# Optimization experiments

Hardware: AMD Instinct MI355X
Metric: run time of the kernel (lower is better)

Reference implementation:

```python
import jax, jax.numpy as jnp
import numpy as np

DEPTH = 4
CODEBOOK_NUM = 2048
CODEBOOK_DIM = 256


def setup_inputs() -> dict:
    key = jax.random.key(0)
    k1, k2 = jax.random.split(key)
    z = jax.random.normal(k1, (32, CODEBOOK_DIM, 32, 32), dtype=jnp.float32)
    # matches nn.init.uniform_(weight, -1/K, 1/K)
    codebook = jax.random.uniform(
        k2, (CODEBOOK_NUM, CODEBOOK_DIM), dtype=jnp.float32,
        minval=-1.0 / CODEBOOK_NUM, maxval=1.0 / CODEBOOK_NUM)
    return {"z": z, "codebook": codebook}


def _quantize(flat_z, codebook):
    # ||z||^2 + ||e||^2 - 2 z.e  -> [N, K]
    dists = (jnp.sum(flat_z ** 2, axis=1, keepdims=True)
             + jnp.sum(codebook ** 2, axis=1)
             - 2.0 * flat_z @ codebook.T)
    indices = jnp.argmin(dists, axis=1)          # [N]
    return codebook[indices], indices            # gather [N, C]


def reference(z, codebook):
    B, C, H, W = z.shape
    K = codebook.shape[0]
    residual = z
    q_list, idx_list = [], []
    for _ in range(DEPTH):
        flat = residual.transpose(0, 2, 3, 1).reshape(-1, C)   # [N, C]
        q_flat, idx = _quantize(flat, codebook)
        q = q_flat.reshape(B, H, W, C).transpose(0, 3, 1, 2)   # [B, C, H, W]
        q_list.append(q)
        idx_list.append(idx)
        residual = residual - q
    # prefix-sum across depth (matches the in-place accumulation loop)
    quantized_cum = jnp.cumsum(jnp.stack(q_list, axis=0), axis=0)  # [D,B,C,H,W]
    q_last = quantized_cum[-1]
    # note: residual here is z_orig - sum_q, so ST term is z_orig - 2*sum_q (faithful)
    quantized_z_st = q_last + jax.lax.stop_gradient(residual - q_last)
    all_idx = jnp.concatenate(idx_list, axis=0)                    # [D*N]
    # mean of one-hot == normalized histogram (avoids [D*N, K] materialization)
    counts = jnp.zeros((K,), dtype=jnp.float32).at[all_idx].add(1.0)
    probs = counts / all_idx.shape[0]
    perplexity = jnp.exp(-jnp.sum(probs * jnp.log(jnp.clip(probs, 1e-10))))
    indices = jnp.stack(idx_list, axis=0)                          # [D, N]
    return quantized_cum, quantized_z_st, indices, perplexity
```

## Files before the change

kernel.cpp:

```cpp
#include <hip/hip_runtime.h>
#include <math.h>

#define BB 32
#define CC 256
#define HWt 1024
#define NN 32768
#define KK 2048
#define RQDEPTH 4
#define CAP 64
#define DELTA 1e-3f

typedef __attribute__((ext_vector_type(8))) short short8;
typedef __attribute__((ext_vector_type(16))) float f32x16;

__device__ __forceinline__ float pw128sq(const float4* __restrict__ a4) {
  float r[8];
  {
    float4 p = a4[0], q = a4[1];
    r[0] = __fmul_rn(p.x, p.x); r[1] = __fmul_rn(p.y, p.y);
    r[2] = __fmul_rn(p.z, p.z); r[3] = __fmul_rn(p.w, p.w);
    r[4] = __fmul_rn(q.x, q.x); r[5] = __fmul_rn(q.y, q.y);
    r[6] = __fmul_rn(q.z, q.z); r[7] = __fmul_rn(q.w, q.w);
  }
  for (int i = 1; i < 16; ++i) {
    float4 p = a4[2 * i], q = a4[2 * i + 1];
    r[0] = __fadd_rn(r[0], __fmul_rn(p.x, p.x));
    r[1] = __fadd_rn(r[1], __fmul_rn(p.y, p.y));
    r[2] = __fadd_rn(r[2], __fmul_rn(p.z, p.z));
    r[3] = __fadd_rn(r[3], __fmul_rn(p.w, p.w));
    r[4] = __fadd_rn(r[4], __fmul_rn(q.x, q.x));
    r[5] = __fadd_rn(r[5], __fmul_rn(q.y, q.y));
    r[6] = __fadd_rn(r[6], __fmul_rn(q.z, q.z));
    r[7] = __fadd_rn(r[7], __fmul_rn(q.w, q.w));
  }
  return __fadd_rn(__fadd_rn(__fadd_rn(r[0], r[1]), __fadd_rn(r[2], r[3])),
                   __fadd_rn(__fadd_rn(r[4], r[5]), __fadd_rn(r[6], r[7])));
}

__device__ __forceinline__ unsigned short f2bf(float x) {
  unsigned u = __float_as_uint(x);
  return (unsigned short)((u + 0x7fffu + ((u >> 16) & 1u)) >> 16);
}
__device__ __forceinline__ unsigned fenc(float f) {
  unsigned u = __float_as_uint(f);
  return (u & 0x80000000u) ? ~u : (u | 0x80000000u);
}
__device__ __forceinline__ float fdec(unsigned k) {
  return __uint_as_float((k & 0x80000000u) ? (k ^ 0x80000000u) : ~k);
}

__global__ void k_ztrans(const float* __restrict__ z, float* __restrict__ resid) {
  __shared__ float tile[32][33];
  int b = blockIdx.z, c0 = blockIdx.y * 32, hw0 = blockIdx.x * 32;
  int tx = threadIdx.x & 31, ty = threadIdx.x >> 5;
  for (int i = ty; i < 32; i += 8)
    tile[i][tx] = z[((size_t)b * CC + c0 + i) * HWt + hw0 + tx];
  __syncthreads();
  for (int i = ty; i < 32; i += 8)
    resid[((size_t)b * HWt + hw0 + i) * CC + c0 + tx] = tile[tx][i];
}

__global__ void k_esplit(const float* __restrict__ cb, short8* __restrict__ esH8,
                         short8* __restrict__ esL8) {
  const int tg = blockIdx.x * 256 + threadIdx.x;
  const int k = tg >> 5, c8 = tg & 31;
  const int idx8 = ((k >> 5) * 32 + c8) * 32 + (k & 31);
  short8 H, L;
#pragma unroll
  for (int i = 0; i < 8; ++i) {
    float x = cb[(size_t)k * CC + c8 * 8 + i];
    unsigned short h = f2bf(x);
    float hf = __uint_as_float(((unsigned)h) << 16);
    unsigned short l = f2bf(__fsub_rn(x, hf));
    H[i] = (short)h; L[i] = (short)l;
  }
  esH8[idx8] = H; esL8[idx8] = L;
}

__global__ void k_bnorm(const float* __restrict__ cb, float* __restrict__ Bcol) {
  int k = blockIdx.x * 256 + threadIdx.x;
  if (k >= KK) return;
  const float4* row = (const float4*)(cb + (size_t)k * CC);
  Bcol[k] = __fadd_rn(pw128sq(row), pw128sq(row + 32));
}

__global__ void k_anorm(const float* __restrict__ resid, float* __restrict__ Arow) {
  int n = blockIdx.x * 256 + threadIdx.x;
  if (n >= NN) return;
  const float4* row = (const float4*)(resid + (size_t)n * CC);
  Arow[n] = __fadd_rn(pw128sq(row), pw128sq(row + 32));
}

__global__ void k_zero(int* counts) {
  int t = blockIdx.x * 256 + threadIdx.x;
  if (t < KK) counts[t] = 0;
}

__global__ __launch_bounds__(512, 4) void k_bulk(
    const float* __restrict__ resid, const short8* __restrict__ esH8,
    const short8* __restrict__ esL8, const float* __restrict__ cb,
    const float* __restrict__ Arow, const float* __restrict__ Bcol,
    int* __restrict__ idxAll, float* __restrict__ idxOut,
    int* __restrict__ counts, int depth) {
  __shared__ short8 zH8[32 * 32];
  __shared__ short8 zL8[32 * 32];
  __shared__ float zf[32 * 260];
  __shared__ int cnt[32];
  __shared__ unsigned minkey[32];
  __shared__ unsigned long long best[32];
  __shared__ int clist[32 * CAP];

  const int t = threadIdx.x;
  const int row0 = blockIdx.x * 32;

  if (t < 32) { cnt[t] = 0; minkey[t] = 0xFFFFFFFFu; best[t] = ~0ull; }

  {
    const int row = t >> 4;
    const int c4b = t & 15;
    const float4* src = (const float4*)(resid + (size_t)(row0 + row) * CC);
#pragma unroll
    for (int g = 0; g < 4; ++g) {
      const int c4i = c4b + 16 * g;
      *(float4*)(zf + row * 260 + c4i * 4) = src[c4i];
    }
  }
  __syncthreads();
  {
    const int srow = t & 31;
    const int c8a = (t >> 5) * 2;
#pragma unroll
    for (int cc = 0; cc < 2; ++cc) {
      const int c8 = c8a + cc;
      short8 H, L;
#pragma unroll
      for (int i = 0; i < 8; ++i) {
        float x = zf[srow * 260 + c8 * 8 + i];
        unsigned short h = f2bf(x);
        float hf = __uint_as_float(((unsigned)h) << 16);
        unsigned short l = f2bf(__fsub_rn(x, hf));
        H[i] = (short)h; L[i] = (short)l;
      }
      zH8[c8 * 32 + srow] = H;
      zL8[c8 * 32 + srow] = L;
    }
  }
  __syncthreads();

  const int wave = t >> 6, lane = t & 63;
  const int l31 = lane & 31, hh = lane >> 5;

#define LOADF(AH, AL, EH, EL, STEP)                                            \
  { const int o_ = ((STEP) * 2 + hh) * 32 + l31;                               \
    AH = zH8[o_]; AL = zL8[o_];                                                \
    EH = esH8[kt * 1024 + o_]; EL = esL8[kt * 1024 + o_]; }

#pragma unroll 1
  for (int it = 0; it < 8; ++it) {
    const int kt = wave * 8 + it, kb = kt * 32;
    f32x16 a0, a1;
#pragma unroll
    for (int i = 0; i < 16; ++i) { a0[i] = 0.f; a1[i] = 0.f; }

    short8 cah, cal, ceh, cel, nah, nal, neh, nel;
    LOADF(cah, cal, ceh, cel, 0)
#pragma unroll
    for (int step = 0; step < 16; ++step) {
      if (step < 15) LOADF(nah, nal, neh, nel, step + 1)
      a0 = __builtin_amdgcn_mfma_f32_32x32x16_bf16(cah, ceh, a0, 0, 0, 0);
      a1 = __builtin_amdgcn_mfma_f32_32x32x16_bf16(cah, cel, a1, 0, 0, 0);
      a1 = __builtin_amdgcn_mfma_f32_32x32x16_bf16(cal, ceh, a1, 0, 0, 0);
      __builtin_amdgcn_sched_barrier(0);
      if (step < 15) { cah = nah; cal = nal; ceh = neh; cel = nel; }
    }

    const float bkv = Bcol[kb + l31];
    float dt[16];
#pragma unroll
    for (int r = 0; r < 16; ++r) {
      const float m = __fadd_rn(a0[r], a1[r]);
      dt[r] = __fsub_rn(bkv, __fadd_rn(m, m));
    }
    if (it == 0) {
#pragma unroll
      for (int r = 0; r < 16; ++r) {
        float rm = dt[r];
#pragma unroll
        for (int m = 1; m < 32; m <<= 1) rm = fminf(rm, __shfl_xor(rm, m));
        if (l31 == 0) {
          const int rowr = (r & 3) + 8 * (r >> 2) + 4 * hh;
          atomicMin(&minkey[rowr], fenc(rm));
        }
      }
    }
#pragma unroll
    for (int r = 0; r < 16; ++r) {
      const int rowr = (r & 3) + 8 * (r >> 2) + 4 * hh;
      const float thr = fdec(minkey[rowr]) + DELTA;
      if (dt[r] <= thr) {
        atomicMin(&minkey[rowr], fenc(dt[r]));
        int idx = atomicAdd(&cnt[rowr], 1);
        if (idx < CAP) clist[rowr * CAP + idx] = kb + l31;
      }
    }
  }
  __syncthreads();

  {
    const int row = t >> 4;
    const int nc0 = cnt[row];
    const int nc = nc0 < CAP ? nc0 : CAP;
    const float av = Arow[row0 + row];
    const float* zr = zf + row * 260;
    for (int s = (t & 15); s < nc; s += 16) {
      const int k = clist[row * CAP + s];
      const float4* e4 = (const float4*)(cb + (size_t)k * CC);
      float a = 0.f;
#pragma unroll 8
      for (int c4 = 0; c4 < 64; ++c4) {
        const float4 z4 = *(const float4*)(zr + c4 * 4);
        const float4 q4 = e4[c4];
        a = fmaf(z4.x, q4.x, a);
        a = fmaf(z4.y, q4.y, a);
        a = fmaf(z4.z, q4.z, a);
        a = fmaf(z4.w, q4.w, a);
      }
      const float Cv = __fadd_rn(av, Bcol[k]);
      const float sv = __fsub_rn(Cv, __fadd_rn(a, a));
      unsigned long long pk =
          ((unsigned long long)__float_as_uint(sv) << 32) | (unsigned)k;
      atomicMin(&best[row], pk);
    }
  }
  __syncthreads();
  if (t < 32) {
    const int wi = (int)(unsigned)(best[t] & 0xffffffffu);
    const int n = row0 + t;
    idxAll[depth * NN + n] = wi;
    idxOut[n] = (float)wi;
    atomicAdd(counts + wi, 1);
  }
}

__global__ void k_update(const float* __restrict__ cb, const int* __restrict__ idxAll,
                         float* __restrict__ resid, float* __restrict__ cum,
                         float* __restrict__ zst, int depth) {
  __shared__ float qt[32][33];
  __shared__ float rt[32][33];
  int b = blockIdx.z, c0 = blockIdx.y * 32, hw0 = blockIdx.x * 32;
  int tx = threadIdx.x & 31, ty = threadIdx.x >> 5;
  const int* idx = idxAll + depth * NN;
  for (int i = ty; i < 32; i += 8) {
    int n = b * HWt + hw0 + i;
    int kk = idx[n];
    size_t fo = (size_t)n * CC + c0 + tx;
    float q = cb[(size_t)kk * CC + c0 + tx];
    float r = __fsub_rn(resid[fo], q);
    resid[fo] = r;
    qt[i][tx] = q;
    rt[i][tx] = r;
  }
  __syncthreads();
  const size_t PLANE = (size_t)NN * CC;
  for (int i = ty; i < 32; i += 8) {
    size_t oo = ((size_t)b * CC + c0 + i) * HWt + hw0 + tx;
    float q = qt[tx][i];
    float prevv = (depth == 0) ? 0.f : cum[(size_t)(depth - 1) * PLANE + oo];
    cum[(size_t)depth * PLANE + oo] = __fadd_rn(prevv, q);
    if (depth == 3) zst[oo] = rt[tx][i];
  }
}

__global__ void k_perp(const int* __restrict__ counts, float* __restrict__ out) {
  __shared__ double sh[256];
  double s = 0.0;
  for (int k = threadIdx.x; k < KK; k += 256) {
    int c = counts[k];
    if (c > 0) {
      double p = (double)c / (double)(RQDEPTH * NN);
      s += p * log(p);
    }
  }
  sh[threadIdx.x] = s;
  __syncthreads();
  for (int st = 128; st; st >>= 1) {
    if (threadIdx.x < st) sh[threadIdx.x] += sh[threadIdx.x + st];
    __syncthreads();
  }
  if (threadIdx.x == 0) out[0] = (float)exp(-sh[0]);
}

extern "C" void kernel_launch(void* const* d_in, const int* in_sizes, int n_in,
                              void* d_out, int out_size, void* d_ws, size_t ws_size,
                              hipStream_t stream) {
  const float* z  = (const float*)d_in[0];
  const float* cb = (const float*)d_in[1];
  float* out = (float*)d_out;
  const size_t PLANE = (size_t)NN * CC;
  float* cum  = out;
  float* zst  = out + (size_t)RQDEPTH * PLANE;
  float* idxo = zst + PLANE;
  float* perp = idxo + (size_t)RQDEPTH * NN;

  float* resid = (float*)d_ws;
  float* esbase = resid + PLANE;
  short8* esH8 = (short8*)esbase;
  short8* esL8 = esH8 + 65536;
  float* Arow  = esbase + (size_t)CC * KK;
  float* Bcol  = Arow + NN;
  int* idxAll  = (int*)(Bcol + KK);
  int* counts  = idxAll + RQDEPTH * NN;

  dim3 tgrid(HWt / 32, CC / 32, BB);
  k_ztrans<<<tgrid, 256, 0, stream>>>(z, resid);
  k_esplit<<<256, 256, 0, stream>>>(cb, esH8, esL8);
  k_bnorm<<<KK / 256, 256, 0, stream>>>(cb, Bcol);
  k_zero<<<(KK + 255) / 256, 256, 0, stream>>>(counts);

  for (int d = 0; d < RQDEPTH; ++d) {
    k_anorm<<<NN / 256, 256, 0, stream>>>(resid, Arow);
    k_bulk<<<NN / 32, 512, 0, stream>>>(resid, esH8, esL8, cb, Arow, Bcol,
                                        idxAll, idxo + (size_t)d * NN, counts, d);
    k_update<<<tgrid, 256, 0, stream>>>(cb, idxAll, resid, cum, zst, d);
  }
  k_perp<<<1, 256, 0, stream>>>(counts, perp);
}
```

Before: 946.4 us.

## Use single bf16 MFMA screening with wider margin and exact fp32 fallback

Drops the hi/lo bf16 split, so the candidate screen runs one bf16 MFMA per step instead of three. The shared-memory fp32 residual copy goes away and refinement reads the residual from global memory. The screening margin is raised to compensate for the coarser precision, and rows that overflow the candidate cap fall back to an exact scan over all codes. LDS shrinks enough to allow 8 blocks per CU. The risks are more candidates to refine per row, occasional full-scan fallbacks, and global-memory reads in the refine loop.

```diff
diff --git a/kernel.cpp b/kernel.cpp
--- a/kernel.cpp
+++ b/kernel.cpp
@@ -8,7 +8,7 @@
 #define KK 2048
 #define RQDEPTH 4
 #define CAP 64
-#define DELTA 1e-3f
+#define DELTA 4e-3f
 
 typedef __attribute__((ext_vector_type(8))) short short8;
 typedef __attribute__((ext_vector_type(16))) float f32x16;
@@ -49,6 +49,21 @@
   return __uint_as_float((k & 0x80000000u) ? (k ^ 0x80000000u) : ~k);
 }
 
+__device__ __forceinline__ float exact_dot(const float4* __restrict__ zr4,
+                                           const float4* __restrict__ e4) {
+  float a = 0.f;
+#pragma unroll 8
+  for (int c4 = 0; c4 < 64; ++c4) {
+    const float4 z4 = zr4[c4];
+    const float4 q4 = e4[c4];
+    a = fmaf(z4.x, q4.x, a);
+    a = fmaf(z4.y, q4.y, a);
+    a = fmaf(z4.z, q4.z, a);
+    a = fmaf(z4.w, q4.w, a);
+  }
+  return a;
+}
+
 __global__ void k_ztrans(const float* __restrict__ z, float* __restrict__ resid) {
   __shared__ float tile[32][33];
   int b = blockIdx.z, c0 = blockIdx.y * 32, hw0 = blockIdx.x * 32;
@@ -60,21 +75,18 @@
     resid[((size_t)b * HWt + hw0 + i) * CC + c0 + tx] = tile[tx][i];
 }
 
-__global__ void k_esplit(const float* __restrict__ cb, short8* __restrict__ esH8,
-                         short8* __restrict__ esL8) {
+__global__ void k_esplitH(const float* __restrict__ cb, short8* __restrict__ esH8) {
   const int tg = blockIdx.x * 256 + threadIdx.x;
   const int k = tg >> 5, c8 = tg & 31;
   const int idx8 = ((k >> 5) * 32 + c8) * 32 + (k & 31);
-  short8 H, L;
-#pragma unroll
-  for (int i = 0; i < 8; ++i) {
-    float x = cb[(size_t)k * CC + c8 * 8 + i];
-    unsigned short h = f2bf(x);
-    float hf = __uint_as_float(((unsigned)h) << 16);
-    unsigned short l = f2bf(__fsub_rn(x, hf));
-    H[i] = (short)h; L[i] = (short)l;
-  }
-  esH8[idx8] = H; esL8[idx8] = L;
+  const float4* s4 = (const float4*)(cb + (size_t)k * CC + c8 * 8);
+  float4 p = s4[0], q = s4[1];
+  short8 H;
+  H[0] = (short)f2bf(p.x); H[1] = (short)f2bf(p.y);
+  H[2] = (short)f2bf(p.z); H[3] = (short)f2bf(p.w);
+  H[4] = (short)f2bf(q.x); H[5] = (short)f2bf(q.y);
+  H[6] = (short)f2bf(q.z); H[7] = (short)f2bf(q.w);
+  esH8[idx8] = H;
 }
 
 __global__ void k_bnorm(const float* __restrict__ cb, float* __restrict__ Bcol) {
@@ -96,15 +108,12 @@
   if (t < KK) counts[t] = 0;
 }
 
-__global__ __launch_bounds__(512, 4) void k_bulk(
+__global__ __launch_bounds__(512, 8) void k_bulk(
     const float* __restrict__ resid, const short8* __restrict__ esH8,
-    const short8* __restrict__ esL8, const float* __restrict__ cb,
-    const float* __restrict__ Arow, const float* __restrict__ Bcol,
-    int* __restrict__ idxAll, float* __restrict__ idxOut,
-    int* __restrict__ counts, int depth) {
+    const float* __restrict__ cb, const float* __restrict__ Arow,
+    const float* __restrict__ Bcol, int* __restrict__ idxAll,
+    float* __restrict__ idxOut, int* __restrict__ counts, int depth) {
   __shared__ short8 zH8[32 * 32];
-  __shared__ short8 zL8[32 * 32];
-  __shared__ float zf[32 * 260];
   __shared__ int cnt[32];
   __shared__ unsigned minkey[32];
   __shared__ unsigned long long best[32];
@@ -116,33 +125,20 @@
   if (t < 32) { cnt[t] = 0; minkey[t] = 0xFFFFFFFFu; best[t] = ~0ull; }
 
   {
-    const int row = t >> 4;
-    const int c4b = t & 15;
-    const float4* src = (const float4*)(resid + (size_t)(row0 + row) * CC);
-#pragma unroll
-    for (int g = 0; g < 4; ++g) {
-      const int c4i = c4b + 16 * g;
-      *(float4*)(zf + row * 260 + c4i * 4) = src[c4i];
-    }
-  }
-  __syncthreads();
-  {
     const int srow = t & 31;
     const int c8a = (t >> 5) * 2;
 #pragma unroll
     for (int cc = 0; cc < 2; ++cc) {
       const int c8 = c8a + cc;
-      short8 H, L;
-#pragma unroll
-      for (int i = 0; i < 8; ++i) {
-        float x = zf[srow * 260 + c8 * 8 + i];
-        unsigned short h = f2bf(x);
-        float hf = __uint_as_float(((unsigned)h) << 16);
-        unsigned short l = f2bf(__fsub_rn(x, hf));
-        H[i] = (short)h; L[i] = (short)l;
-      }
+      const float4* s4 =
+          (const float4*)(resid + (size_t)(row0 + srow) * CC + c8 * 8);
+      float4 p = s4[0], q = s4[1];
+      short8 H;
+      H[0] = (short)f2bf(p.x); H[1] = (short)f2bf(p.y);
+      H[2] = (short)f2bf(p.z); H[3] = (short)f2bf(p.w);
+      H[4] = (short)f2bf(q.x); H[5] = (short)f2bf(q.y);
+      H[6] = (short)f2bf(q.z); H[7] = (short)f2bf(q.w);
       zH8[c8 * 32 + srow] = H;
-      zL8[c8 * 32 + srow] = L;
     }
   }
   __syncthreads();
@@ -150,35 +146,32 @@
   const int wave = t >> 6, lane = t & 63;
   const int l31 = lane & 31, hh = lane >> 5;
 
-#define LOADF(AH, AL, EH, EL, STEP)                                            \
+#define LOADF(AH, EH, STEP)                                                    \
   { const int o_ = ((STEP) * 2 + hh) * 32 + l31;                               \
-    AH = zH8[o_]; AL = zL8[o_];                                                \
-    EH = esH8[kt * 1024 + o_]; EL = esL8[kt * 1024 + o_]; }
+    AH = zH8[o_]; EH = esH8[kt * 1024 + o_]; }
 
 #pragma unroll 1
   for (int it = 0; it < 8; ++it) {
     const int kt = wave * 8 + it, kb = kt * 32;
-    f32x16 a0, a1;
-#pragma unroll
-    for (int i = 0; i < 16; ++i) { a0[i] = 0.f; a1[i] = 0.f; }
-
-    short8 cah, cal, ceh, cel, nah, nal, neh, nel;
-    LOADF(cah, cal, ceh, cel, 0)
+    f32x16 a0;
+#pragma unroll
+    for (int i = 0; i < 16; ++i) a0[i] = 0.f;
+
+    short8 cah, ceh, nah, neh;
+    LOADF(cah, ceh, 0)
 #pragma unroll
     for (int step = 0; step < 16; ++step) {
-      if (step < 15) LOADF(nah, nal, neh, nel, step + 1)
+      if (step < 15) LOADF(nah, neh, step + 1)
       a0 = __builtin_amdgcn_mfma_f32_32x32x16_bf16(cah, ceh, a0, 0, 0, 0);
-      a1 = __builtin_amdgcn_mfma_f32_32x32x16_bf16(cah, cel, a1, 0, 0, 0);
-      a1 = __builtin_amdgcn_mfma_f32_32x32x16_bf16(cal, ceh, a1, 0, 0, 0);
       __builtin_amdgcn_sched_barrier(0);
-      if (step < 15) { cah = nah; cal = nal; ceh = neh; cel = nel; }
+      if (step < 15) { cah = nah; ceh = neh; }
     }
 
     const float bkv = Bcol[kb + l31];
     float dt[16];
 #pragma unroll
     for (int r = 0; r < 16; ++r) {
-      const float m = __fadd_rn(a0[r], a1[r]);
+      const float m = a0[r];
       dt[r] = __fsub_rn(bkv, __fadd_rn(m, m));
     }
     if (it == 0) {
@@ -209,27 +202,27 @@
   {
     const int row = t >> 4;
     const int nc0 = cnt[row];
-    const int nc = nc0 < CAP ? nc0 : CAP;
     const float av = Arow[row0 + row];
-    const float* zr = zf + row * 260;
-    for (int s = (t & 15); s < nc; s += 16) {
-      const int k = clist[row * CAP + s];
-      const float4* e4 = (const float4*)(cb + (size_t)k * CC);
-      float a = 0.f;
-#pragma unroll 8
-      for (int c4 = 0; c4 < 64; ++c4) {
-        const float4 z4 = *(const float4*)(zr + c4 * 4);
-        const float4 q4 = e4[c4];
-        a = fmaf(z4.x, q4.x, a);
-        a = fmaf(z4.y, q4.y, a);
-        a = fmaf(z4.z, q4.z, a);
-        a = fmaf(z4.w, q4.w, a);
+    const float4* zr4 = (const float4*)(resid + (size_t)(row0 + row) * CC);
+    if (nc0 <= CAP) {
+      for (int s = (t & 15); s < nc0; s += 16) {
+        const int k = clist[row * CAP + s];
+        const float a = exact_dot(zr4, (const float4*)(cb + (size_t)k * CC));
+        const float Cv = __fadd_rn(av, Bcol[k]);
+        const float sv = __fsub_rn(Cv, __fadd_rn(a, a));
+        unsigned long long pk =
+            ((unsigned long long)__float_as_uint(sv) << 32) | (unsigned)k;
+        atomicMin(&best[row], pk);
       }
-      const float Cv = __fadd_rn(av, Bcol[k]);
-      const float sv = __fsub_rn(Cv, __fadd_rn(a, a));
-      unsigned long long pk =
-          ((unsigned long long)__float_as_uint(sv) << 32) | (unsigned)k;
-      atomicMin(&best[row], pk);
+    } else {
+      for (int k = (t & 15); k < KK; k += 16) {
+        const float a = exact_dot(zr4, (const float4*)(cb + (size_t)k * CC));
+        const float Cv = __fadd_rn(av, Bcol[k]);
+        const float sv = __fsub_rn(Cv, __fadd_rn(a, a));
+        unsigned long long pk =
+            ((unsigned long long)__float_as_uint(sv) << 32) | (unsigned)k;
+        atomicMin(&best[row], pk);
+      }
     }
   }
   __syncthreads();
@@ -305,7 +298,6 @@
   float* resid = (float*)d_ws;
   float* esbase = resid + PLANE;
   short8* esH8 = (short8*)esbase;
-  short8* esL8 = esH8 + 65536;
   float* Arow  = esbase + (size_t)CC * KK;
   float* Bcol  = Arow + NN;
   int* idxAll  = (int*)(Bcol + KK);
@@ -313,13 +305,13 @@
 
   dim3 tgrid(HWt / 32, CC / 32, BB);
   k_ztrans<<<tgrid, 256, 0, stream>>>(z, resid);
-  k_esplit<<<256, 256, 0, stream>>>(cb, esH8, esL8);
+  k_esplitH<<<256, 256, 0, stream>>>(cb, esH8);
   k_bnorm<<<KK / 256, 256, 0, stream>>>(cb, Bcol);
   k_zero<<<(KK + 255) / 256, 256, 0, stream>>>(counts);
 
   for (int d = 0; d < RQDEPTH; ++d) {
     k_anorm<<<NN / 256, 256, 0, stream>>>(resid, Arow);
-    k_bulk<<<NN / 32, 512, 0, stream>>>(resid, esH8, esL8, cb, Arow, Bcol,
+    k_bulk<<<NN / 32, 512, 0, stream>>>(resid, esH8, cb, Arow, Bcol,
                                         idxAll, idxo + (size_t)d * NN, counts, d);
     k_update<<<tgrid, 256, 0, stream>>>(cb, idxAll, resid, cum, zst, d);
   }
```

Measured after the change: 969.7 us. 1.02x slower.
